# Optimization experiments

Hardware: AMD Instinct MI355X
Metric: run time of the kernel (lower is better)

The kernel has to match this reference:

```python
import jax, jax.numpy as jnp
import numpy as np

K = 3           # kernel_size
PAD = 1         # padding
HEADS = 6
C = 192
CH = C // HEADS           # channels per head = 32
SCALE = CH ** (-0.5)
KK = K * K                # 9


def unfold3(x):
    # x: [N,C,H,W] -> [N,C,9,H,W] (im2col with k=3, pad=1, stride=1)
    N, c, H, W = x.shape
    xp = jnp.pad(x, ((0, 0), (0, 0), (PAD, PAD), (PAD, PAD)))
    return jnp.stack([xp[:, :, i:i + H, j:j + W] for i in range(K) for j in range(K)], axis=2)


def fold3(y):
    # y: [N,C,9,H,W] -> [N,C,H,W] (scatter-add inverse of unfold3)
    N, c, kk, H, W = y.shape
    out = jnp.zeros((N, c, H + 2 * PAD, W + 2 * PAD), dtype=y.dtype)
    idx = 0
    for i in range(K):
        for j in range(K):
            out = out.at[:, :, i:i + H, j:j + W].add(y[:, :, idx])
            idx += 1
    return out[:, :, PAD:PAD + H, PAD:PAD + W]


def setup_inputs() -> dict:
    key = jax.random.key(0)
    ks = jax.random.split(key, 6)
    N, H, W = 16, 56, 56
    s = 0.02
    return {
        "x": jax.random.normal(ks[0], (N, C, H, W), jnp.float32),
        "Wv": jax.random.normal(ks[1], (C, C), jnp.float32) * s,          # fc (no bias)
        "Wa": jax.random.normal(ks[2], (C, KK * KK * HEADS), jnp.float32) * s,  # fc_att weight
        "ba": jax.random.normal(ks[3], (KK * KK * HEADS,), jnp.float32) * s,
        "Wp": jax.random.normal(ks[4], (C, C), jnp.float32) * s,          # fc_proj weight
        "bp": jax.random.normal(ks[5], (C,), jnp.float32) * s,
    }


def reference(x, Wv, Wa, ba, Wp, bp):
    N, c, H, W = x.shape
    HW = H * W
    # value projection (pointwise linear over channels)
    v = jnp.einsum("nchw,cd->ndhw", x, Wv)
    # unfold values: [N,C,9,H,W] -> [N,heads,ch,9,HW] -> [N,heads,HW,9,ch]
    vu = unfold3(v).reshape(N, HEADS, CH, KK, HW).transpose(0, 1, 4, 3, 2)
    # attention logits from (avg-pooled, here identity since stride=1) input
    att = jnp.einsum("nchw,ck->nhwk", x, Wa) + ba       # [N,H,W,81*heads]
    att = att.reshape(N, HW, HEADS, KK, KK).transpose(0, 2, 1, 3, 4)  # [N,heads,HW,9,9]
    att = jax.nn.softmax(att * SCALE, axis=-1)          # dropout is identity at inference
    # apply per-position 9x9 attention to the 9 gathered neighbors
    out = jnp.einsum("nhpkl,nhplc->nhpkc", att, vu)      # [N,heads,HW,9,ch]
    # fold back: layout (heads, ch, kk) matches unfold layout (C, kk)
    out = out.transpose(0, 1, 4, 3, 2).reshape(N, c, KK, H, W)
    folded = fold3(out)                                  # [N,C,H,W]
    # output projection
    return jnp.einsum("nchw,cd->ndhw", folded, Wp) + bp[None, :, None, None]
```

## Files before the change

kernel.cpp:

```cpp
#include <hip/hip_runtime.h>
#include <hip/hip_bf16.h>
#include <math.h>

#define HW 3136
#define NC 192
#define NHEADS 6
#define IMG 56
#define NATT 486
#define YSTR 768
#define ATT_SCALE 0.17677669529663687f

typedef __attribute__((ext_vector_type(8))) short short8;
typedef __attribute__((ext_vector_type(8))) unsigned short ushort8;
typedef __attribute__((ext_vector_type(4))) float float4v;

__device__ __forceinline__ float bf2f(unsigned short u) {
    unsigned int x = ((unsigned int)u) << 16;
    return __builtin_bit_cast(float, x);
}
__device__ __forceinline__ unsigned short f2bf(float f) {
    __hip_bfloat16 h = __float2bfloat16(f);
    return __builtin_bit_cast(unsigned short, h);
}
__device__ __forceinline__ void gload_lds16(const void* g, void* l) {
    __builtin_amdgcn_global_load_lds((const __attribute__((address_space(1))) void*)g,
                                     (__attribute__((address_space(3))) void*)l, 16, 0, 0);
}

__global__ __launch_bounds__(256) void transpose_x(const float* __restrict__ x,
                                                   unsigned short* __restrict__ xt)
{
    __shared__ float tile[64][65];
    int bx = blockIdx.x;
    int n = (bx * 64) / HW;
    int hw0 = (bx * 64) % HW;
    int c0 = blockIdx.y * 64;
    int tl = threadIdx.x & 63, tg = threadIdx.x >> 6;
    const float* xn = x + (size_t)n * NC * HW;
#pragma unroll
    for (int i = 0; i < 16; ++i)
        tile[tg * 16 + i][tl] = xn[(size_t)(c0 + tg * 16 + i) * HW + hw0 + tl];
    __syncthreads();
    unsigned short* xp = xt + ((size_t)n * HW + hw0) * NC + c0;
#pragma unroll
    for (int i = 0; i < 16; ++i) {
        int hwr = tg * 16 + i;
        xp[(size_t)hwr * NC + tl] = f2bf(tile[tl][hwr]);
    }
}

__global__ __launch_bounds__(256) void prep_weights(
    const float* __restrict__ Wv, const float* __restrict__ Wa, const float* __restrict__ Wp,
    const float* __restrict__ ba,
    unsigned short* __restrict__ Wall, unsigned short* __restrict__ Wpt,
    float* __restrict__ ball)
{
    int idx = blockIdx.x * 256 + threadIdx.x;
    if (idx < 36864) {
        int d = idx / 192, k = idx - d * 192;
        Wpt[idx] = f2bf(Wp[(size_t)k * NC + d]);
    }
    if (idx < 147456) {
        int d = idx / 192, k = idx - d * 192;
        unsigned short val;
        float bv = 0.f;
        if (d < 192) {
            val = f2bf(Wv[(size_t)k * NC + d]);
        } else {
            int dp = d - 192;
            int head = dp / 96, rr = dp - head * 96;
            int k9 = rr / 10, l = rr - k9 * 10;
            bool valid = (k9 < 9) && (l < 9);
            int src = head * 81 + k9 * 9 + l;
            val = valid ? f2bf(Wa[(size_t)k * NATT + src]) : (unsigned short)0;
            bv = valid ? ba[src] : 0.f;
        }
        Wall[idx] = val;
        if (k == 0) ball[d] = bv;
    }
}

__global__ __launch_bounds__(256) void gemm_big(
    const unsigned short* __restrict__ A, const unsigned short* __restrict__ W,
    const float* __restrict__ ball, unsigned short* __restrict__ Y)
{
    __shared__ __align__(16) unsigned short As[2][4096];
    __shared__ __align__(16) unsigned short Bs[2][4096];
    int t = threadIdx.x, lane = t & 63, wave = t >> 6;
    int col0 = blockIdx.x * 128, row0 = blockIdx.y * 128;
    int fr = lane & 15, fq = lane >> 4;
    int wm = (wave >> 1) * 64, wn = (wave & 1) * 64;
    int srow = lane >> 2;
    int soff = (lane & 3) * 16;
    const char* Ab = (const char*)A;
    const char* Wb = (const char*)W;

    float4v acc[4][4] = {};

#define STAGE_BIG(buf, k0)                                                        \
    {                                                                             \
        _Pragma("unroll")                                                         \
        for (int i = 0; i < 2; ++i) {                                             \
            int j = wave * 2 + i;                                                 \
            gload_lds16(Ab + (size_t)(row0 + j * 16 + srow) * 384 + (k0)*2 + soff,\
                        (char*)As[buf] + j * 1024);                               \
            gload_lds16(Wb + (size_t)(col0 + j * 16 + srow) * 384 + (k0)*2 + soff,\
                        (char*)Bs[buf] + j * 1024);                               \
        }                                                                         \
    }

    STAGE_BIG(0, 0);
    for (int s = 0; s < 6; ++s) {
        if (s < 5) STAGE_BIG((s + 1) & 1, (s + 1) * 32);
        __syncthreads();
        int buf = s & 1;
        short8 af[4], bf[4];
#pragma unroll
        for (int mi = 0; mi < 4; ++mi)
            af[mi] = *(const short8*)((const char*)As[buf] + (wm + mi * 16 + fr) * 64 + fq * 16);
#pragma unroll
        for (int ni = 0; ni < 4; ++ni)
            bf[ni] = *(const short8*)((const char*)Bs[buf] + (wn + ni * 16 + fr) * 64 + fq * 16);
#pragma unroll
        for (int mi = 0; mi < 4; ++mi)
#pragma unroll
            for (int ni = 0; ni < 4; ++ni)
                acc[mi][ni] = __builtin_amdgcn_mfma_f32_16x16x32_bf16(
                    af[mi], bf[ni], acc[mi][ni], 0, 0, 0);
        __syncthreads();
    }

#pragma unroll
    for (int ni = 0; ni < 4; ++ni) {
        int col = col0 + wn + ni * 16 + fr;
        float b = ball[col];
#pragma unroll
        for (int mi = 0; mi < 4; ++mi) {
            int row = row0 + wm + mi * 16 + fq * 4;
#pragma unroll
            for (int r = 0; r < 4; ++r)
                Y[(size_t)(row + r) * YSTR + col] = f2bf(acc[mi][ni][r] + b);
        }
    }
#undef STAGE_BIG
}

__global__ __launch_bounds__(256) void gemm_small(
    const unsigned short* __restrict__ A,
    const unsigned short* __restrict__ B,
    const float* __restrict__ bias, float* __restrict__ out)
{
    __shared__ __align__(16) unsigned short As[2][2048];
    __shared__ __align__(16) unsigned short Bs[2][8192];
    int t = threadIdx.x, lane = t & 63, wave = t >> 6;
    int n0 = blockIdx.x * 256, m0 = blockIdx.y * 64;
    int fr = lane & 15, fq = lane >> 4;
    int srow = lane >> 2, soff = (lane & 3) * 16;
    const char* Ab = (const char*)A;
    const char* Bb = (const char*)B;

    float4v acc[4][4] = {};

#define STAGE_SMALL(buf, k0)                                                      \
    {                                                                             \
        gload_lds16(Ab + (size_t)(m0 + wave * 16 + srow) * 384 + (k0)*2 + soff,   \
                    (char*)As[buf] + wave * 1024);                                \
        _Pragma("unroll")                                                         \
        for (int i = 0; i < 4; ++i) {                                             \
            int j = wave * 4 + i;                                                 \
            gload_lds16(Bb + (size_t)(n0 + j * 16 + srow) * 384 + (k0)*2 + soff,  \
                        (char*)Bs[buf] + j * 1024);                               \
        }                                                                         \
    }

    STAGE_SMALL(0, 0);
    for (int s = 0; s < 6; ++s) {
        if (s < 5) STAGE_SMALL((s + 1) & 1, (s + 1) * 32);
        __syncthreads();
        int buf = s & 1;
        short8 af[4], bf[4];
#pragma unroll
        for (int mi = 0; mi < 4; ++mi)
            af[mi] = *(const short8*)((const char*)As[buf] + (mi * 16 + fr) * 64 + fq * 16);
#pragma unroll
        for (int ni = 0; ni < 4; ++ni)
            bf[ni] = *(const short8*)((const char*)Bs[buf] + (wave * 64 + ni * 16 + fr) * 64 + fq * 16);
#pragma unroll
        for (int mi = 0; mi < 4; ++mi)
#pragma unroll
            for (int ni = 0; ni < 4; ++ni)
                acc[mi][ni] = __builtin_amdgcn_mfma_f32_16x16x32_bf16(
                    af[mi], bf[ni], acc[mi][ni], 0, 0, 0);
        __syncthreads();
    }

#pragma unroll
    for (int ni = 0; ni < 4; ++ni) {
        int n = n0 + wave * 64 + ni * 16 + fr;
        int img = n / HW, phw = n - img * HW;
        float* op = out + (size_t)img * (NC * HW) + phw;
#pragma unroll
        for (int mi = 0; mi < 4; ++mi) {
            int m = m0 + mi * 16 + fq * 4;
#pragma unroll
            for (int r = 0; r < 4; ++r)
                op[(size_t)(m + r) * HW] = acc[mi][ni][r] + bias[m + r];
        }
    }
#undef STAGE_SMALL
}

__global__ __launch_bounds__(256, 4) void fused_att_agg(
    const unsigned short* __restrict__ Y, unsigned short* __restrict__ fold)
{
    __shared__ __align__(16) char vt[25600];
    int t = threadIdx.x;
    int bid = blockIdx.x;
    int head = bid % NHEADS; int tmp = bid / NHEADS;
    int tcol = tmp & 1; tmp >>= 1;
    int trow = tmp % 7; int img = tmp / 7;
    int h0 = trow * 8, w0 = tcol * 28;

    const unsigned short* Yv = Y + head * 32;
    ushort8 stg[6];
#pragma unroll
    for (int i = 0; i < 6; ++i) {
        int u = i * 256 + t;
        int slot = u >> 2, q = u & 3;
        int vrow = slot >> 5, vcol = slot & 31;
        int hh = h0 - 2 + vrow, ww = w0 - 2 + vcol;
        bool ok = (hh >= 0) & (hh < IMG) & (ww >= 0) & (ww < IMG);
        int hc = min(max(hh, 0), IMG - 1);
        int wcl = min(max(ww, 0), IMG - 1);
        ushort8 val = *(const ushort8*)(Yv + (size_t)(img * HW + hc * IMG + wcl) * YSTR + q * 8);
        if (!ok) val = (ushort8){};
        stg[i] = val;
    }

    int ph = t / 28, pw = t - (t / 28) * 28;
    int h = h0 + ph, w = w0 + pw;
    float wc[25];
#pragma unroll
    for (int d = 0; d < 25; ++d) wc[d] = 0.f;
    if (t < 224) {
        const unsigned short* Yatt = Y + 192 + head * 96;
#pragma unroll
        for (int k = 0; k < 9; ++k) {
            const int oky = k / 3 - 1, okx = k % 3 - 1;
            int hh = h - oky, ww = w - okx;
            bool ok = (hh >= 0) & (hh < IMG) & (ww >= 0) & (ww < IMG);
            int hc = min(max(hh, 0), IMG - 1);
            int wcl = min(max(ww, 0), IMG - 1);
            const unsigned short* ap =
                Yatt + (size_t)(img * HW + hc * IMG + wcl) * YSTR + k * 10;
            ushort8 a8;
            __builtin_memcpy(&a8, ap, 16);
            float a[9];
#pragma unroll
            for (int l = 0; l < 8; ++l) a[l] = bf2f(a8[l]);
            a[8] = bf2f(ap[8]);
            float m = -1e30f;
#pragma unroll
            for (int l = 0; l < 9; ++l) m = fmaxf(m, a[l]);
            float s = 0.f;
#pragma unroll
            for (int l = 0; l < 9; ++l) {
                a[l] = __expf((a[l] - m) * ATT_SCALE);
                s += a[l];
            }
            float g = ok ? (1.f / s) : 0.f;
#pragma unroll
            for (int l = 0; l < 9; ++l) {
                const int dy = (l / 3 - 1) - oky + 2;
                const int dx = (l % 3 - 1) - okx + 2;
                wc[dy * 5 + dx] += a[l] * g;
            }
        }
    }

#pragma unroll
    for (int i = 0; i < 6; ++i) {
        int u = i * 256 + t;
        int slot = u >> 2, q = u & 3;
        *(ushort8*)(vt + q * 6400 + slot * 16) = stg[i];
    }
    __syncthreads();

    if (t < 224) {
        int base = (ph * 32 + pw) * 16;
        int pos = img * HW + h * IMG + w;
        unsigned short* fo = fold + (size_t)pos * NC + head * 32;
#pragma unroll
        for (int q = 0; q < 4; ++q) {
            const char* vq = vt + q * 6400 + base;
            float acc[8];
#pragma unroll
            for (int j = 0; j < 8; ++j) acc[j] = 0.f;
#pragma unroll
            for (int d = 0; d < 25; ++d) {
                const int dy = d / 5, dx = d % 5;
                float wf = wc[d];
                ushort8 vv = *(const ushort8*)(vq + dy * 512 + dx * 16);
#pragma unroll
                for (int j = 0; j < 8; ++j)
                    acc[j] += wf * bf2f(vv[j]);
            }
            ushort8 ov;
#pragma unroll
            for (int j = 0; j < 8; ++j) ov[j] = f2bf(acc[j]);
            *(ushort8*)(fo + q * 8) = ov;
        }
    }
}

extern "C" void kernel_launch(void* const* d_in, const int* in_sizes, int n_in,
                              void* d_out, int out_size, void* d_ws, size_t ws_size,
                              hipStream_t stream)
{
    const float* x  = (const float*)d_in[0];
    const float* Wv = (const float*)d_in[1];
    const float* Wa = (const float*)d_in[2];
    const float* ba = (const float*)d_in[3];
    const float* Wp = (const float*)d_in[4];
    const float* bp = (const float*)d_in[5];
    float* out = (float*)d_out;

    unsigned short* xt    = (unsigned short*)d_ws;
    unsigned short* Y     = xt + 9633792;
    unsigned short* Wall  = Y + 38535168;
    unsigned short* Wpt   = Wall + 147456;
    float*          ball  = (float*)(Wpt + 36864);
    unsigned short* foldb = xt;

    dim3 blk(256);
    prep_weights<<<576, blk, 0, stream>>>(Wv, Wa, Wp, ba, Wall, Wpt, ball);
    transpose_x<<<dim3(784, 3), blk, 0, stream>>>(x, xt);
    gemm_big<<<dim3(6, 392), blk, 0, stream>>>(xt, Wall, ball, Y);
    fused_att_agg<<<1344, blk, 0, stream>>>(Y, foldb);
    gemm_small<<<dim3(196, 3), blk, 0, stream>>>(Wpt, foldb, bp, out);
}
```

Baseline: 195.2 us.

## Split GEMM output into head-major V and compact attention buffers

The big GEMM epilogue now writes value channels into a head-major [head][pos][32] buffer and attention logits into a compact [head*9+k][pos][10] buffer, dropping the padded 768-wide Y rows and the padding columns. The aggregation kernel reads contiguous per-head data, which should give better locality and less traffic. It also pads the LDS tile row stride from 32 to 36 slots to reduce bank conflicts, and unpacks bf16 pairs from 32-bit words. The GEMM epilogue stores become strided scatter writes (stride 32 or 10 elements), which may coalesce worse.

```diff
diff --git a/kernel.cpp b/kernel.cpp
--- a/kernel.cpp
+++ b/kernel.cpp
@@ -3,20 +3,27 @@
 #include <math.h>
 
 #define HW 3136
+#define NPOS 50176
 #define NC 192
 #define NHEADS 6
 #define IMG 56
 #define NATT 486
-#define YSTR 768
 #define ATT_SCALE 0.17677669529663687f
 
 typedef __attribute__((ext_vector_type(8))) short short8;
 typedef __attribute__((ext_vector_type(8))) unsigned short ushort8;
 typedef __attribute__((ext_vector_type(4))) float float4v;
+typedef __attribute__((ext_vector_type(4))) unsigned int uint4v;
 
 __device__ __forceinline__ float bf2f(unsigned short u) {
     unsigned int x = ((unsigned int)u) << 16;
     return __builtin_bit_cast(float, x);
+}
+__device__ __forceinline__ float bf2f_lo(unsigned int u) {
+    return __builtin_bit_cast(float, u << 16);
+}
+__device__ __forceinline__ float bf2f_hi(unsigned int u) {
+    return __builtin_bit_cast(float, u & 0xffff0000u);
 }
 __device__ __forceinline__ unsigned short f2bf(float f) {
     __hip_bfloat16 h = __float2bfloat16(f);
@@ -82,7 +89,8 @@
 
 __global__ __launch_bounds__(256) void gemm_big(
     const unsigned short* __restrict__ A, const unsigned short* __restrict__ W,
-    const float* __restrict__ ball, unsigned short* __restrict__ Y)
+    const float* __restrict__ ball,
+    unsigned short* __restrict__ Vo, unsigned short* __restrict__ ATo)
 {
     __shared__ __align__(16) unsigned short As[2][4096];
     __shared__ __align__(16) unsigned short Bs[2][4096];
@@ -134,12 +142,30 @@
     for (int ni = 0; ni < 4; ++ni) {
         int col = col0 + wn + ni * 16 + fr;
         float b = ball[col];
+        unsigned short* bptr;
+        size_t rstr;
+        bool valid;
+        if (col < 192) {
+            int hd = col >> 5, ch = col & 31;
+            bptr = Vo + ((size_t)hd * NPOS) * 32 + ch;
+            rstr = 32;
+            valid = true;
+        } else {
+            int dp = col - 192;
+            int hd = dp / 96, rr = dp - hd * 96;
+            int k9 = rr / 10, l = rr - k9 * 10;
+            valid = (k9 < 9);
+            bptr = ATo + ((size_t)(hd * 9 + (k9 < 9 ? k9 : 8)) * NPOS) * 10 + l;
+            rstr = 10;
+        }
 #pragma unroll
         for (int mi = 0; mi < 4; ++mi) {
             int row = row0 + wm + mi * 16 + fq * 4;
 #pragma unroll
-            for (int r = 0; r < 4; ++r)
-                Y[(size_t)(row + r) * YSTR + col] = f2bf(acc[mi][ni][r] + b);
+            for (int r = 0; r < 4; ++r) {
+                unsigned short val = f2bf(acc[mi][ni][r] + b);
+                if (valid) bptr[(size_t)(row + r) * rstr] = val;
+            }
         }
     }
 #undef STAGE_BIG
@@ -211,9 +237,10 @@
 }
 
 __global__ __launch_bounds__(256, 4) void fused_att_agg(
-    const unsigned short* __restrict__ Y, unsigned short* __restrict__ fold)
-{
-    __shared__ __align__(16) char vt[25600];
+    const unsigned short* __restrict__ V, const unsigned short* __restrict__ AT,
+    unsigned short* __restrict__ fold)
+{
+    __shared__ __align__(16) char vt[4 * 434 * 16];
     int t = threadIdx.x;
     int bid = blockIdx.x;
     int head = bid % NHEADS; int tmp = bid / NHEADS;
@@ -221,7 +248,7 @@
     int trow = tmp % 7; int img = tmp / 7;
     int h0 = trow * 8, w0 = tcol * 28;
 
-    const unsigned short* Yv = Y + head * 32;
+    const unsigned short* Vh = V + (size_t)head * NPOS * 32;
     ushort8 stg[6];
 #pragma unroll
     for (int i = 0; i < 6; ++i) {
@@ -232,7 +259,7 @@
         bool ok = (hh >= 0) & (hh < IMG) & (ww >= 0) & (ww < IMG);
         int hc = min(max(hh, 0), IMG - 1);
         int wcl = min(max(ww, 0), IMG - 1);
-        ushort8 val = *(const ushort8*)(Yv + (size_t)(img * HW + hc * IMG + wcl) * YSTR + q * 8);
+        ushort8 val = *(const ushort8*)(Vh + (size_t)(img * HW + hc * IMG + wcl) * 32 + q * 8);
         if (!ok) val = (ushort8){};
         stg[i] = val;
     }
@@ -243,7 +270,7 @@
 #pragma unroll
     for (int d = 0; d < 25; ++d) wc[d] = 0.f;
     if (t < 224) {
-        const unsigned short* Yatt = Y + 192 + head * 96;
+        int head9 = head * 9;
 #pragma unroll
         for (int k = 0; k < 9; ++k) {
             const int oky = k / 3 - 1, okx = k % 3 - 1;
@@ -251,14 +278,13 @@
             bool ok = (hh >= 0) & (hh < IMG) & (ww >= 0) & (ww < IMG);
             int hc = min(max(hh, 0), IMG - 1);
             int wcl = min(max(ww, 0), IMG - 1);
-            const unsigned short* ap =
-                Yatt + (size_t)(img * HW + hc * IMG + wcl) * YSTR + k * 10;
-            ushort8 a8;
-            __builtin_memcpy(&a8, ap, 16);
-            float a[9];
-#pragma unroll
-            for (int l = 0; l < 8; ++l) a[l] = bf2f(a8[l]);
-            a[8] = bf2f(ap[8]);
+            size_t nidx = (size_t)img * HW + hc * IMG + wcl;
+            const unsigned int* ap32 =
+                (const unsigned int*)(AT + ((size_t)(head9 + k) * NPOS + nidx) * 10);
+            unsigned int u0 = ap32[0], u1 = ap32[1], u2 = ap32[2], u3 = ap32[3], u4 = ap32[4];
+            float a[9] = { bf2f_lo(u0), bf2f_hi(u0), bf2f_lo(u1), bf2f_hi(u1),
+                           bf2f_lo(u2), bf2f_hi(u2), bf2f_lo(u3), bf2f_hi(u3),
+                           bf2f_lo(u4) };
             float m = -1e30f;
 #pragma unroll
             for (int l = 0; l < 9; ++l) m = fmaxf(m, a[l]);
@@ -282,17 +308,18 @@
     for (int i = 0; i < 6; ++i) {
         int u = i * 256 + t;
         int slot = u >> 2, q = u & 3;
-        *(ushort8*)(vt + q * 6400 + slot * 16) = stg[i];
+        int vrow = slot >> 5, vcol = slot & 31;
+        *(ushort8*)(vt + q * (434 * 16) + (vrow * 36 + vcol) * 16) = stg[i];
     }
     __syncthreads();
 
     if (t < 224) {
-        int base = (ph * 32 + pw) * 16;
+        int base = (ph * 36 + pw) * 16;
         int pos = img * HW + h * IMG + w;
         unsigned short* fo = fold + (size_t)pos * NC + head * 32;
 #pragma unroll
         for (int q = 0; q < 4; ++q) {
-            const char* vq = vt + q * 6400 + base;
+            const char* vq = vt + q * (434 * 16) + base;
             float acc[8];
 #pragma unroll
             for (int j = 0; j < 8; ++j) acc[j] = 0.f;
@@ -300,10 +327,12 @@
             for (int d = 0; d < 25; ++d) {
                 const int dy = d / 5, dx = d % 5;
                 float wf = wc[d];
-                ushort8 vv = *(const ushort8*)(vq + dy * 512 + dx * 16);
-#pragma unroll
-                for (int j = 0; j < 8; ++j)
-                    acc[j] += wf * bf2f(vv[j]);
+                uint4v vv = *(const uint4v*)(vq + (dy * 36 + dx) * 16);
+#pragma unroll
+                for (int z = 0; z < 4; ++z) {
+                    acc[2 * z]     += wf * bf2f_lo(vv[z]);
+                    acc[2 * z + 1] += wf * bf2f_hi(vv[z]);
+                }
             }
             ushort8 ov;
 #pragma unroll
@@ -325,17 +354,18 @@
     const float* bp = (const float*)d_in[5];
     float* out = (float*)d_out;
 
-    unsigned short* xt    = (unsigned short*)d_ws;
-    unsigned short* Y     = xt + 9633792;
-    unsigned short* Wall  = Y + 38535168;
-    unsigned short* Wpt   = Wall + 147456;
-    float*          ball  = (float*)(Wpt + 36864);
+    unsigned short* xt   = (unsigned short*)d_ws;
+    unsigned short* V    = xt + 9633792;
+    unsigned short* AT   = V + 9633792;
+    unsigned short* Wall = AT + 27095040;
+    unsigned short* Wpt  = Wall + 147456;
+    float*          ball = (float*)(Wpt + 36864);
     unsigned short* foldb = xt;
 
     dim3 blk(256);
     prep_weights<<<576, blk, 0, stream>>>(Wv, Wa, Wp, ba, Wall, Wpt, ball);
     transpose_x<<<dim3(784, 3), blk, 0, stream>>>(x, xt);
-    gemm_big<<<dim3(6, 392), blk, 0, stream>>>(xt, Wall, ball, Y);
-    fused_att_agg<<<1344, blk, 0, stream>>>(Y, foldb);
+    gemm_big<<<dim3(6, 392), blk, 0, stream>>>(xt, Wall, ball, V, AT);
+    fused_att_agg<<<1344, blk, 0, stream>>>(V, AT, foldb);
     gemm_small<<<dim3(196, 3), blk, 0, stream>>>(Wpt, foldb, bp, out);
 }
```

Result: no change. 192.3 us (-1.5%).
